# Kernel tuning notes

Measured on AMD Instinct MI355X. Metric: run time of the kernel, lower is better.

The kernel has to match this reference:

```python
import jax, jax.numpy as jnp
import numpy as np
import math

B, T, D, DA = 4, 4096, 1024, 64
N_LAYERS = 12  # scaling uses sqrt(DA) * 12 per the original module


def setup_inputs() -> dict:
    key = jax.random.key(0)
    ks = jax.random.split(key, 7)
    s = 1.0 / math.sqrt(D)
    return {
        "x": jax.random.normal(ks[0], (B, T, D), dtype=jnp.float32),
        "Wq": jax.random.normal(ks[1], (D, DA), dtype=jnp.float32) * s,
        "bq": jax.random.normal(ks[2], (DA,), dtype=jnp.float32) * 0.01,
        "Wk": jax.random.normal(ks[3], (D, DA), dtype=jnp.float32) * s,
        "bk": jax.random.normal(ks[4], (DA,), dtype=jnp.float32) * 0.01,
        "Wv": jax.random.normal(ks[5], (D, DA), dtype=jnp.float32) * s,
        "bv": jax.random.normal(ks[6], (DA,), dtype=jnp.float32) * 0.01,
    }


def reference(x, Wq, bq, Wk, bk, Wv, bv):
    # x: [B, T, D]
    q = jnp.einsum('btd,da->bta', x, Wq) + bq  # [B, T, DA]
    k = jnp.einsum('btd,da->bta', x, Wk) + bk
    v = jnp.einsum('btd,da->bta', x, Wv) + bv
    scale = 1.0 / (math.sqrt(DA) * N_LAYERS)
    scores = jnp.einsum('bqa,bka->bqk', q, k) * scale  # [B, T, T]
    causal = jnp.tril(jnp.ones((T, T), dtype=bool))
    scores = jnp.where(causal[None, :, :], scores, -jnp.inf)
    attn = jax.nn.softmax(scores, axis=-1)
    return jnp.einsum('bqk,bka->bqa', attn, v)  # [B, T, DA]
```

## Files before the change

kernel.cpp:

```cpp
#include <hip/hip_runtime.h>
#include <hip/hip_bf16.h>


#define T_SEQ 4096
#define NW 12

using bf16x8 = __bf16 __attribute__((ext_vector_type(8)));
using f32x16 = float __attribute__((ext_vector_type(16)));
using uint4v = unsigned int __attribute__((ext_vector_type(4)));

static constexpr float QSCALE = 1.4426950408889634f / 96.0f;

__device__ __forceinline__ unsigned short bf1(float v) {
    unsigned u = __builtin_bit_cast(unsigned, v);
    u += 0x7FFFu + ((u >> 16) & 1u);
    return (unsigned short)(u >> 16);
}
__device__ __forceinline__ unsigned cvt2(float lo, float hi) {
    unsigned r;
    asm("v_cvt_pk_bf16_f32 %0, %1, %2" : "=v"(r) : "v"(lo), "v"(hi));
    return r;
}
__device__ __forceinline__ void pswap(unsigned& a, unsigned& b) {
    asm volatile("v_permlane32_swap_b32 %0, %1" : "+v"(a), "+v"(b));
}
__device__ __forceinline__ float bflo(unsigned u) {
    return __builtin_bit_cast(float, u << 16);
}
__device__ __forceinline__ float bfhi(unsigned u) {
    return __builtin_bit_cast(float, u & 0xFFFF0000u);
}
__device__ __forceinline__ f32x16 zero16() {
    f32x16 z;
#pragma unroll
    for (int i = 0; i < 16; ++i) z[i] = 0.0f;
    return z;
}
#define MFMA32(a, b, c) __builtin_amdgcn_mfma_f32_32x32x16_bf16(a, b, c, 0, 0, 0)

__global__ __launch_bounds__(256) void prep_w(
        const float* __restrict__ Wq, const float* __restrict__ Wk,
        const float* __restrict__ Wv, const float* __restrict__ bq,
        const float* __restrict__ bk, const float* __restrict__ bv,
        unsigned short* __restrict__ Wt3, float* __restrict__ bias_t) {
    __shared__ float tile[64][65];
    const int tid = threadIdx.x;
    const int m = blockIdx.x >> 4, kt = blockIdx.x & 15, d0 = kt * 64;
    const float* W = (m == 0) ? Wq : (m == 1) ? Wk : Wv;
    const int a = tid & 63, r4 = tid >> 6;
#pragma unroll
    for (int j = 0; j < 16; ++j) {
        const int rr = r4 + 4 * j;
        tile[rr][a] = W[(size_t)(d0 + rr) * 64 + a];
    }
    __syncthreads();
    const float scl = (m == 0) ? QSCALE : 1.0f;
    const int dc = tid & 63, ar = tid >> 6;
#pragma unroll
    for (int j = 0; j < 16; ++j) {
        const int aa = ar + 4 * j;
        const int cg = m * 64 + aa;
        const size_t addr =
            ((size_t)(kt * 6 + (cg >> 5)) * 4 + (dc >> 4)) * 512 +
            ((cg & 31) + 32 * ((dc >> 3) & 1)) * 8 + (dc & 7);
        Wt3[addr] = bf1(tile[dc][aa] * scl);
    }
    if (kt == 0 && tid < 64) {
        const float* bb = (m == 0) ? bq : (m == 1) ? bk : bv;
        bias_t[m * 64 + tid] = bb[tid] * scl;
    }
}

__global__ __launch_bounds__(384, 3) void proj_kernel(
        const float* __restrict__ x, const unsigned short* __restrict__ Wt3,
        const float* __restrict__ bias_t, unsigned short* __restrict__ qs,
        unsigned short* __restrict__ ksf, unsigned short* __restrict__ vtf) {
    __shared__ unsigned short Ald[2][32 * 68];

    const int tid = threadIdx.x;
    const int w = tid >> 6, l = tid & 63, g = l >> 5, c32 = l & 31;
    const int ct = w;
    const int rowbase = blockIdx.x * 32;

    const int r0 = tid >> 4, k40 = tid & 15;
    const int r1 = (tid + 384) >> 4, k41 = tid & 15;
    const bool haveB = (tid < 128);
    const float* xb0 = x + (size_t)(rowbase + r0) * 1024 + k40 * 4;
    const float* xb1 = x + (size_t)(rowbase + r1) * 1024 + k41 * 4;
    const int wo0 = r0 * 68 + k40 * 4;
    const int wo1 = r1 * 68 + k41 * 4;

    const unsigned short* Wb = Wt3 + (size_t)(ct * 4) * 512 + l * 8;
    const int aro = c32 * 68;

    f32x16 acc = zero16();
    float4 ra[3], rb[3];

    {
        float4 a0 = *(const float4*)(xb0);
        float4 b0;
        if (haveB) b0 = *(const float4*)(xb1);
        *(uint2*)(Ald[0] + wo0) = make_uint2(cvt2(a0.x, a0.y), cvt2(a0.z, a0.w));
        if (haveB)
            *(uint2*)(Ald[0] + wo1) = make_uint2(cvt2(b0.x, b0.y), cvt2(b0.z, b0.w));
    }
#pragma unroll
    for (int s = 1; s <= 3; ++s) {
        ra[s % 3] = *(const float4*)(xb0 + s * 64);
        if (haveB) rb[s % 3] = *(const float4*)(xb1 + s * 64);
    }
    asm volatile("s_waitcnt lgkmcnt(0)" ::: "memory");
    __builtin_amdgcn_s_barrier();
    __builtin_amdgcn_sched_barrier(0);

#pragma unroll
    for (int kt = 0; kt < 16; ++kt) {
        const unsigned short* A = Ald[kt & 1];
        const unsigned short* Wkt = Wb + (size_t)kt * 12288;
        bf16x8 b0 = *(const bf16x8*)(Wkt);
        bf16x8 b1 = *(const bf16x8*)(Wkt + 512);
        bf16x8 b2 = *(const bf16x8*)(Wkt + 1024);
        bf16x8 b3 = *(const bf16x8*)(Wkt + 1536);
        if (kt < 15) {
            float4 a = ra[(kt + 1) % 3];
            *(uint2*)(Ald[(kt + 1) & 1] + wo0) =
                make_uint2(cvt2(a.x, a.y), cvt2(a.z, a.w));
            if (haveB) {
                float4 b4 = rb[(kt + 1) % 3];
                *(uint2*)(Ald[(kt + 1) & 1] + wo1) =
                    make_uint2(cvt2(b4.x, b4.y), cvt2(b4.z, b4.w));
            }
        }
        if (kt < 12) {
            ra[(kt + 4) % 3] = *(const float4*)(xb0 + (kt + 4) * 64);
            if (haveB) rb[(kt + 4) % 3] = *(const float4*)(xb1 + (kt + 4) * 64);
        }
        {
            bf16x8 a0 = *(const bf16x8*)(A + aro + (0 + g) * 8);
            bf16x8 a1 = *(const bf16x8*)(A + aro + (2 + g) * 8);
            bf16x8 a2 = *(const bf16x8*)(A + aro + (4 + g) * 8);
            bf16x8 a3 = *(const bf16x8*)(A + aro + (6 + g) * 8);
            acc = MFMA32(a0, b0, acc);
            acc = MFMA32(a1, b1, acc);
            acc = MFMA32(a2, b2, acc);
            acc = MFMA32(a3, b3, acc);
        }
        asm volatile("s_waitcnt lgkmcnt(0)" ::: "memory");
        __builtin_amdgcn_s_barrier();
        __builtin_amdgcn_sched_barrier(0);
    }

    const int cg = ct * 32 + c32;
    const float bias = bias_t[cg];
    const int mat = cg >> 6, cm = cg & 63;
    if (mat == 2) {
#pragma unroll
        for (int q4 = 0; q4 < 4; ++q4) {
            const int rowg = rowbase + 8 * q4 + 4 * g;
            const int b = rowg >> 12, tl = rowg & (T_SEQ - 1);
            const int ch = tl >> 5;
            const int f = (cm >> 5) * 2 + (q4 >> 1);
            const int lane = (cm & 31) + 32 * (q4 & 1);
            unsigned lo = cvt2(acc[4 * q4 + 0] + bias, acc[4 * q4 + 1] + bias);
            unsigned hi = cvt2(acc[4 * q4 + 2] + bias, acc[4 * q4 + 3] + bias);
            *(uint2*)(vtf + ((size_t)b * 128 + ch) * 2048 + f * 512 +
                      lane * 8 + 4 * g) = make_uint2(lo, hi);
        }
    } else if (mat == 1) {
#pragma unroll
        for (int r = 0; r < 16; ++r) {
            const int rowg = rowbase + (r & 3) + 8 * (r >> 2) + 4 * g;
            const int b = rowg >> 12, tl = rowg & (T_SEQ - 1);
            ksf[((size_t)b * 128 + (tl >> 5)) * 2048 + (cm >> 4) * 512 +
                ((tl & 31) + 32 * ((cm >> 3) & 1)) * 8 + (cm & 7)] =
                bf1(acc[r] + bias);
        }
    } else {
#pragma unroll
        for (int r = 0; r < 16; ++r) {
            const int rowg = rowbase + (r & 3) + 8 * (r >> 2) + 4 * g;
            qs[(size_t)rowg * 64 + cm] = bf1(acc[r] + bias);
        }
    }
}

__global__ __launch_bounds__(768, 3) void attn_kernel(
        const unsigned short* __restrict__ qs, const unsigned short* __restrict__ ksf,
        const unsigned short* __restrict__ vtf, float* __restrict__ out) {
    __shared__ unsigned short Osh[NW][32][66];
    __shared__ float msh[NW][32];
    __shared__ float ssh[NW][32];

    const int tid = threadIdx.x;
    const int w = tid >> 6, l = tid & 63, g = l >> 5, c32 = l & 31;
    const int b = blockIdx.x & 3;
    const int pid = blockIdx.x >> 2;

    for (int tt = 0; tt < 2; ++tt) {
        const int jt = tt ? pid : 127 - pid;
        const int qbase = jt * 32;

        const unsigned short* qp =
            qs + ((size_t)b * T_SEQ + qbase + c32) * 64 + g * 8;
        bf16x8 qf[4];
#pragma unroll
        for (int t = 0; t < 4; ++t) qf[t] = *(const bf16x8*)(qp + 16 * t);

        const unsigned short* pKc = ksf + ((size_t)b * 128 + w) * 2048 + l * 8;
        const unsigned short* pVc = vtf + ((size_t)b * 128 + w) * 2048 + l * 8;

        auto loadK = [&](bf16x8(&kf)[4]) {
#pragma unroll
            for (int t = 0; t < 4; ++t)
                kf[t] = *(const bf16x8*)(pKc + t * 512);
            pKc += NW * 2048;
        };
        auto loadV = [&](bf16x8(&vf)[4]) {
#pragma unroll
            for (int f = 0; f < 4; ++f)
                vf[f] = *(const bf16x8*)(pVc + f * 512);
            pVc += NW * 2048;
        };

        const int nch = (jt >= w) ? (jt - w) / NW + 1 : 0;
        const bool hasDiag = (jt >= w) && ((jt - w) % NW == 0);
        float m = -INFINITY, ssum = 0.0f;
        f32x16 o0 = zero16(), o1 = zero16();
        f32x16 s_cur;
        bf16x8 k0[4], k1[4], vR[4];

        if (nch > 0) {
            loadK(k0);
            f32x16 t = zero16();
#pragma unroll
            for (int t4 = 0; t4 < 4; ++t4) t = MFMA32(k0[t4], qf[t4], t);
            s_cur = t;
        }

        auto STEP = [&](bf16x8(&kn)[4], int i) {
            loadV(vR);
            if (i + 1 < nch) loadK(kn);
            if (hasDiag && i == nch - 1) {
#pragma unroll
                for (int r = 0; r < 16; ++r) {
                    const int kl = (r & 3) + 8 * (r >> 2) + 4 * g;
                    if (kl > c32) s_cur[r] = -1e30f;
                }
            }
            float a0 = fmaxf(fmaxf(s_cur[0], s_cur[1]), fmaxf(s_cur[2], s_cur[3]));
            float a1 = fmaxf(fmaxf(s_cur[4], s_cur[5]), fmaxf(s_cur[6], s_cur[7]));
            float a2 = fmaxf(fmaxf(s_cur[8], s_cur[9]), fmaxf(s_cur[10], s_cur[11]));
            float a3 = fmaxf(fmaxf(s_cur[12], s_cur[13]), fmaxf(s_cur[14], s_cur[15]));
            float pm = fmaxf(fmaxf(a0, a1), fmaxf(a2, a3));
            if (!__all(pm <= m + 8.0f)) {
                float rmax = fmaxf(pm, __shfl_xor(pm, 32, 64));
                const float mn = fmaxf(m, rmax);
                const float alpha = exp2f(m - mn);
#pragma unroll
                for (int r = 0; r < 16; ++r) { o0[r] *= alpha; o1[r] *= alpha; }
                ssum *= alpha;
                m = mn;
            }
            float p[16];
#pragma unroll
            for (int r = 0; r < 16; ++r) p[r] = exp2f(s_cur[r] - m);
            float s0 = (p[0] + p[1]) + (p[2] + p[3]);
            float s1 = (p[4] + p[5]) + (p[6] + p[7]);
            float s2 = (p[8] + p[9]) + (p[10] + p[11]);
            float s3 = (p[12] + p[13]) + (p[14] + p[15]);
            ssum += (s0 + s1) + (s2 + s3);
            unsigned c01 = cvt2(p[0], p[1]), c23 = cvt2(p[2], p[3]);
            unsigned c45 = cvt2(p[4], p[5]), c67 = cvt2(p[6], p[7]);
            pswap(c01, c45); pswap(c23, c67);
            unsigned c89 = cvt2(p[8], p[9]), cab = cvt2(p[10], p[11]);
            unsigned ccd = cvt2(p[12], p[13]), cef = cvt2(p[14], p[15]);
            pswap(c89, ccd); pswap(cab, cef);
            uint4v u0; u0[0] = c01; u0[1] = c23; u0[2] = c45; u0[3] = c67;
            uint4v u1; u1[0] = c89; u1[1] = cab; u1[2] = ccd; u1[3] = cef;
            bf16x8 pb0 = __builtin_bit_cast(bf16x8, u0);
            bf16x8 pb1 = __builtin_bit_cast(bf16x8, u1);
            __builtin_amdgcn_s_setprio(1);
            o0 = MFMA32(vR[0], pb0, o0);
            o0 = MFMA32(vR[1], pb1, o0);
            o1 = MFMA32(vR[2], pb0, o1);
            o1 = MFMA32(vR[3], pb1, o1);
            if (i + 1 < nch) {
                f32x16 t = zero16();
#pragma unroll
                for (int t4 = 0; t4 < 4; ++t4) t = MFMA32(kn[t4], qf[t4], t);
                s_cur = t;
            }
            __builtin_amdgcn_s_setprio(0);
        };

        int i = 0;
        while (i < nch) {
            STEP(k1, i); ++i;
            if (i < nch) { STEP(k0, i); ++i; }
        }
        ssum += __shfl_xor(ssum, 32, 64);

        if (l < 32) { msh[w][l] = m; ssh[w][l] = ssum; }
#pragma unroll
        for (int q4 = 0; q4 < 4; ++q4) {
            const int base = 8 * q4 + 4 * g;
            *(unsigned*)&Osh[w][c32][base]      = cvt2(o0[4 * q4], o0[4 * q4 + 1]);
            *(unsigned*)&Osh[w][c32][base + 2]  = cvt2(o0[4 * q4 + 2], o0[4 * q4 + 3]);
            *(unsigned*)&Osh[w][c32][base + 32] = cvt2(o1[4 * q4], o1[4 * q4 + 1]);
            *(unsigned*)&Osh[w][c32][base + 34] = cvt2(o1[4 * q4 + 2], o1[4 * q4 + 3]);
        }
        __syncthreads();

        if (tid < 512) {
            const int qrow = tid >> 4, e4 = tid & 15;
            float M = -INFINITY;
            float mw[NW];
#pragma unroll
            for (int u = 0; u < NW; ++u) { mw[u] = msh[u][qrow]; M = fmaxf(M, mw[u]); }
            float den = 0.0f;
            float r0 = 0.f, r1 = 0.f, r2 = 0.f, r3 = 0.f;
#pragma unroll
            for (int u = 0; u < NW; ++u) {
                const float scu = exp2f(mw[u] - M);
                den += ssh[u][qrow] * scu;
                const unsigned ua = *(const unsigned*)&Osh[u][qrow][4 * e4];
                const unsigned ub = *(const unsigned*)&Osh[u][qrow][4 * e4 + 2];
                r0 += bflo(ua) * scu;
                r1 += bfhi(ua) * scu;
                r2 += bflo(ub) * scu;
                r3 += bfhi(ub) * scu;
            }
            const float inv = 1.0f / den;
            float4 st;
            st.x = r0 * inv; st.y = r1 * inv; st.z = r2 * inv; st.w = r3 * inv;
            *(float4*)(out + ((size_t)b * T_SEQ + qbase + qrow) * 64 + 4 * e4) = st;
        }
        __syncthreads();
    }
}

extern "C" void kernel_launch(void* const* d_in, const int* in_sizes, int n_in,
                              void* d_out, int out_size, void* d_ws, size_t ws_size,
                              hipStream_t stream) {
    const float* x  = (const float*)d_in[0];
    const float* Wq = (const float*)d_in[1];
    const float* bq = (const float*)d_in[2];
    const float* Wk = (const float*)d_in[3];
    const float* bk = (const float*)d_in[4];
    const float* Wv = (const float*)d_in[5];
    const float* bv = (const float*)d_in[6];
    float* out = (float*)d_out;

    char* ws = (char*)d_ws;
    unsigned short* Wt3    = (unsigned short*)(ws);
    float*          bias_t = (float*)(ws + 393216);
    unsigned short* qsb    = (unsigned short*)(ws + (1u << 20));
    unsigned short* ksb    = (unsigned short*)(ws + (3u << 20));
    unsigned short* vtb    = (unsigned short*)(ws + (5u << 20));

    prep_w<<<48, 256, 0, stream>>>(Wq, Wk, Wv, bq, bk, bv, Wt3, bias_t);
    proj_kernel<<<512, 384, 0, stream>>>(x, Wt3, bias_t, qsb, ksb, vtb);
    attn_kernel<<<256, 768, 0, stream>>>(qsb, ksb, vtb, out);
}
```

Measured before the change: 58.81 us.

## Stream x tiles into LDS via direct global_load_lds with XOR swizzle

The projection kernel now copies fp32 x tiles straight from global memory into a double-buffered LDS buffer with global_load_lds, and uses an XOR swizzle on 16-byte chunks to avoid bank conflicts. Before, each thread staged x through registers, converted to bf16 and wrote it to LDS, with a three-deep register prefetch. The bf16 conversion now happens when the MFMA operands are read from LDS. This frees registers and removes VALU work from the load path. In exchange, the LDS footprint doubles, each tile is read as fp32, and prefetch depth drops to one tile.

```diff
diff --git a/kernel.cpp b/kernel.cpp
--- a/kernel.cpp
+++ b/kernel.cpp
@@ -37,6 +37,12 @@
     return z;
 }
 #define MFMA32(a, b, c) __builtin_amdgcn_mfma_f32_32x32x16_bf16(a, b, c, 0, 0, 0)
+
+__device__ __forceinline__ void gload_lds16(const float* g, float* l) {
+    __builtin_amdgcn_global_load_lds(
+        (const __attribute__((address_space(1))) float*)g,
+        (__attribute__((address_space(3))) float*)l, 16, 0, 0);
+}
 
 __global__ __launch_bounds__(256) void prep_w(
         const float* __restrict__ Wq, const float* __restrict__ Wk,
@@ -75,79 +81,53 @@
         const float* __restrict__ x, const unsigned short* __restrict__ Wt3,
         const float* __restrict__ bias_t, unsigned short* __restrict__ qs,
         unsigned short* __restrict__ ksf, unsigned short* __restrict__ vtf) {
-    __shared__ unsigned short Ald[2][32 * 68];
+    __shared__ float Ald[2][2048];
 
     const int tid = threadIdx.x;
     const int w = tid >> 6, l = tid & 63, g = l >> 5, c32 = l & 31;
     const int ct = w;
     const int rowbase = blockIdx.x * 32;
 
-    const int r0 = tid >> 4, k40 = tid & 15;
-    const int r1 = (tid + 384) >> 4, k41 = tid & 15;
-    const bool haveB = (tid < 128);
-    const float* xb0 = x + (size_t)(rowbase + r0) * 1024 + k40 * 4;
-    const float* xb1 = x + (size_t)(rowbase + r1) * 1024 + k41 * 4;
-    const int wo0 = r0 * 68 + k40 * 4;
-    const int wo1 = r1 * 68 + k41 * 4;
+    const int j1 = w;
+    const int row1 = 4 * j1 + (l >> 4);
+    const float* gp1 = x + (size_t)(rowbase + row1) * 1024 +
+                       (((l & 15) ^ (row1 & 7)) << 2);
+    const bool has2 = (w < 2);
+    const int j2 = 6 + w;
+    const int row2 = 4 * j2 + (l >> 4);
+    const float* gp2 = x + (size_t)(rowbase + row2) * 1024 +
+                       (((l & 15) ^ (row2 & 7)) << 2);
 
     const unsigned short* Wb = Wt3 + (size_t)(ct * 4) * 512 + l * 8;
-    const int aro = c32 * 68;
 
     f32x16 acc = zero16();
-    float4 ra[3], rb[3];
-
-    {
-        float4 a0 = *(const float4*)(xb0);
-        float4 b0;
-        if (haveB) b0 = *(const float4*)(xb1);
-        *(uint2*)(Ald[0] + wo0) = make_uint2(cvt2(a0.x, a0.y), cvt2(a0.z, a0.w));
-        if (haveB)
-            *(uint2*)(Ald[0] + wo1) = make_uint2(cvt2(b0.x, b0.y), cvt2(b0.z, b0.w));
-    }
-#pragma unroll
-    for (int s = 1; s <= 3; ++s) {
-        ra[s % 3] = *(const float4*)(xb0 + s * 64);
-        if (haveB) rb[s % 3] = *(const float4*)(xb1 + s * 64);
-    }
-    asm volatile("s_waitcnt lgkmcnt(0)" ::: "memory");
-    __builtin_amdgcn_s_barrier();
-    __builtin_amdgcn_sched_barrier(0);
+
+    gload_lds16(gp1, &Ald[0][j1 * 256]);
+    if (has2) gload_lds16(gp2, &Ald[0][j2 * 256]);
+    __syncthreads();
 
 #pragma unroll
     for (int kt = 0; kt < 16; ++kt) {
-        const unsigned short* A = Ald[kt & 1];
+        if (kt < 15) {
+            gload_lds16(gp1 + (kt + 1) * 64, &Ald[(kt + 1) & 1][j1 * 256]);
+            if (has2)
+                gload_lds16(gp2 + (kt + 1) * 64, &Ald[(kt + 1) & 1][j2 * 256]);
+        }
+        const float* A = Ald[kt & 1];
         const unsigned short* Wkt = Wb + (size_t)kt * 12288;
-        bf16x8 b0 = *(const bf16x8*)(Wkt);
-        bf16x8 b1 = *(const bf16x8*)(Wkt + 512);
-        bf16x8 b2 = *(const bf16x8*)(Wkt + 1024);
-        bf16x8 b3 = *(const bf16x8*)(Wkt + 1536);
-        if (kt < 15) {
-            float4 a = ra[(kt + 1) % 3];
-            *(uint2*)(Ald[(kt + 1) & 1] + wo0) =
-                make_uint2(cvt2(a.x, a.y), cvt2(a.z, a.w));
-            if (haveB) {
-                float4 b4 = rb[(kt + 1) % 3];
-                *(uint2*)(Ald[(kt + 1) & 1] + wo1) =
-                    make_uint2(cvt2(b4.x, b4.y), cvt2(b4.z, b4.w));
-            }
-        }
-        if (kt < 12) {
-            ra[(kt + 4) % 3] = *(const float4*)(xb0 + (kt + 4) * 64);
-            if (haveB) rb[(kt + 4) % 3] = *(const float4*)(xb1 + (kt + 4) * 64);
-        }
-        {
-            bf16x8 a0 = *(const bf16x8*)(A + aro + (0 + g) * 8);
-            bf16x8 a1 = *(const bf16x8*)(A + aro + (2 + g) * 8);
-            bf16x8 a2 = *(const bf16x8*)(A + aro + (4 + g) * 8);
-            bf16x8 a3 = *(const bf16x8*)(A + aro + (6 + g) * 8);
-            acc = MFMA32(a0, b0, acc);
-            acc = MFMA32(a1, b1, acc);
-            acc = MFMA32(a2, b2, acc);
-            acc = MFMA32(a3, b3, acc);
-        }
-        asm volatile("s_waitcnt lgkmcnt(0)" ::: "memory");
-        __builtin_amdgcn_s_barrier();
-        __builtin_amdgcn_sched_barrier(0);
+#pragma unroll
+        for (int kk = 0; kk < 4; ++kk) {
+            const int blk = kk * 4 + g * 2;
+            float4 f0 = *(const float4*)(A + c32 * 64 + ((blk ^ (c32 & 7)) << 2));
+            float4 f1 = *(const float4*)(A + c32 * 64 + (((blk + 1) ^ (c32 & 7)) << 2));
+            uint4v ua;
+            ua[0] = cvt2(f0.x, f0.y); ua[1] = cvt2(f0.z, f0.w);
+            ua[2] = cvt2(f1.x, f1.y); ua[3] = cvt2(f1.z, f1.w);
+            bf16x8 af = __builtin_bit_cast(bf16x8, ua);
+            bf16x8 bfr = *(const bf16x8*)(Wkt + kk * 512);
+            acc = MFMA32(af, bfr, acc);
+        }
+        __syncthreads();
     }
 
     const int cg = ct * 32 + c32;
```

New measurement: 50.17 us. 1.17x faster.
